# Optimization experiments

Hardware: AMD Instinct MI355X
Metric: run time of the kernel (lower is better)

## Reference

```python
import jax, jax.numpy as jnp
import numpy as np

N_USER = 200_000
N_ITEM = 100_000
E = 1_000_000
HID = 64
ED = 16      # edge_dim
DU = 128     # user feature dim
DI = 64      # item feature dim
NCONV = 4    # 2 layers x (fwd, rev)


def setup_inputs() -> dict:
    key = jax.random.key(0)
    ks = jax.random.split(key, 20)
    s = 0.1  # small init scale for numerical sanity
    return {
        'x_user': jax.random.normal(ks[0], (N_USER, DU), jnp.float32),
        'x_item': jax.random.normal(ks[1], (N_ITEM, DI), jnp.float32),
        'edge_attr': jax.random.normal(ks[2], (E, ED), jnp.float32),
        'src_idx': jax.random.randint(ks[3], (E,), 0, N_USER),
        'dst_idx': jax.random.randint(ks[4], (E,), 0, N_ITEM),
        # input projections
        'Wp_user': jax.random.normal(ks[5], (DU, HID), jnp.float32) * s,
        'bp_user': jnp.zeros((HID,), jnp.float32),
        'Wp_item': jax.random.normal(ks[6], (DI, HID), jnp.float32) * s,
        'bp_item': jnp.zeros((HID,), jnp.float32),
        # per-conv params, stacked over NCONV = [layer0 fwd, layer0 rev, layer1 fwd, layer1 rev]
        'eps': jnp.zeros((NCONV,), jnp.float32),  # train_eps=True, init 0
        'We': jax.random.normal(ks[7], (NCONV, ED, HID), jnp.float32) * s,
        'be': jnp.zeros((NCONV, HID), jnp.float32),
        'W1': jax.random.normal(ks[8], (NCONV, HID, HID), jnp.float32) * s,
        'b1': jnp.zeros((NCONV, HID), jnp.float32),
        'W2': jax.random.normal(ks[9], (NCONV, HID, HID), jnp.float32) * s,
        'b2': jnp.zeros((NCONV, HID), jnp.float32),
    }


def _gine(x_src, x_dst, e_src, e_dst, ea, eps, We, be, W1, b1, W2, b2):
    # GINEConv: out = MLP((1+eps)*x_dst + sum_j ReLU(x_src[j] + Lin(edge_attr_j)))
    msg = jax.nn.relu(x_src[e_src] + ea @ We + be)                 # [E, HID]
    agg = jax.ops.segment_sum(msg, e_dst, num_segments=x_dst.shape[0])
    h = (1.0 + eps) * x_dst + agg
    return jax.nn.relu(h @ W1 + b1) @ W2 + b2


def reference(x_user, x_item, edge_attr, src_idx, dst_idx,
              Wp_user, bp_user, Wp_item, bp_item,
              eps, We, be, W1, b1, W2, b2):
    h_u = jax.nn.relu(x_user @ Wp_user + bp_user)   # [N_USER, HID]
    h_i = jax.nn.relu(x_item @ Wp_item + bp_item)   # [N_ITEM, HID]
    for l in range(2):
        cf, cr = 2 * l, 2 * l + 1
        # fwd relation user->item (dst = item); rev = flipped edges, same edge_attr
        new_i = jax.nn.relu(_gine(h_u, h_i, src_idx, dst_idx, edge_attr,
                                  eps[cf], We[cf], be[cf], W1[cf], b1[cf], W2[cf], b2[cf]))
        new_u = jax.nn.relu(_gine(h_i, h_u, dst_idx, src_idx, edge_attr,
                                  eps[cr], We[cr], be[cr], W1[cr], b1[cr], W2[cr], b2[cr]))
        if l > 0:  # use_residual and not first layer
            h_u, h_i = h_u + new_u, h_i + new_i
        else:
            h_u, h_i = new_u, new_i
    return h_u, h_i
```

## Files before the change

kernel.cpp:

```cpp
#include <hip/hip_runtime.h>
#include <hip/hip_bf16.h>

typedef __hip_bfloat16 bf16;

#define N_USER 200000
#define N_ITEM 100000
#define NEDGE  1000000
#define HID    64

__device__ __forceinline__ float bf2f(unsigned int u) {
    unsigned int x = u << 16;
    float f; __builtin_memcpy(&f, &x, 4); return f;
}
__device__ __forceinline__ float ldf(const void* p, long i, int isf32) {
    if (isf32) return ((const float*)p)[i];
    return bf2f(((const unsigned short*)p)[i]);
}
__device__ __forceinline__ void stf(void* p, long i, int isf32, float v) {
    if (isf32) ((float*)p)[i] = v;
    else       ((bf16*)p)[i] = (bf16)v;
}
__device__ __forceinline__ void load_row16(const void* ea, long e, int isf32, float* v) {
    if (isf32) {
        const float4* p = (const float4*)((const float*)ea + e * 16);
        float4 a = p[0], b = p[1], c = p[2], d = p[3];
        v[0]=a.x; v[1]=a.y; v[2]=a.z; v[3]=a.w;
        v[4]=b.x; v[5]=b.y; v[6]=b.z; v[7]=b.w;
        v[8]=c.x; v[9]=c.y; v[10]=c.z; v[11]=c.w;
        v[12]=d.x; v[13]=d.y; v[14]=d.z; v[15]=d.w;
    } else {
        const int4* q = (const int4*)((const unsigned short*)ea + e * 16);
        int4 s0 = q[0], s1 = q[1];
        unsigned int w;
        w=(unsigned)s0.x; v[0]=bf2f(w & 0xffff); v[1]=bf2f(w >> 16);
        w=(unsigned)s0.y; v[2]=bf2f(w & 0xffff); v[3]=bf2f(w >> 16);
        w=(unsigned)s0.z; v[4]=bf2f(w & 0xffff); v[5]=bf2f(w >> 16);
        w=(unsigned)s0.w; v[6]=bf2f(w & 0xffff); v[7]=bf2f(w >> 16);
        w=(unsigned)s1.x; v[8]=bf2f(w & 0xffff); v[9]=bf2f(w >> 16);
        w=(unsigned)s1.y; v[10]=bf2f(w & 0xffff); v[11]=bf2f(w >> 16);
        w=(unsigned)s1.z; v[12]=bf2f(w & 0xffff); v[13]=bf2f(w >> 16);
        w=(unsigned)s1.w; v[14]=bf2f(w & 0xffff); v[15]=bf2f(w >> 16);
    }
}

__global__ void detect_kernel(const void* __restrict__ x, int* __restrict__ flag) {
    if (threadIdx.x == 0 && blockIdx.x == 0) {
        const unsigned short* p = (const unsigned short*)x;
        int f = 0;
        for (int i = 0; i < 512; i++) {
            int ex = (p[i] >> 7) & 0xFF;
            if (ex >= 137) f = 1;
        }
        *flag = f;
    }
}

__global__ __launch_bounds__(256) void hist_kernel(
    const int* __restrict__ key, int* __restrict__ cnt, int E)
{
    int e = blockIdx.x * 256 + threadIdx.x;
    if (e < E) atomicAdd(&cnt[key[e]], 1);
}

__global__ __launch_bounds__(1024) void scan_kernel(
    const int* __restrict__ deg, int* __restrict__ rowptr,
    int* __restrict__ cursor, int N)
{
    __shared__ int ssum[1024];
    __shared__ int s_carry;
    int tid = threadIdx.x;
    if (tid == 0) s_carry = 0;
    __syncthreads();
    for (int base = 0; base < N; base += 8192) {
        int i0 = base + tid * 8;
        int v[8]; int tot = 0;
#pragma unroll
        for (int k = 0; k < 8; k++) { int i = i0 + k; v[k] = (i < N) ? deg[i] : 0; tot += v[k]; }
        ssum[tid] = tot;
        __syncthreads();
        for (int off = 1; off < 1024; off <<= 1) {
            int t = (tid >= off) ? ssum[tid - off] : 0;
            __syncthreads();
            ssum[tid] += t;
            __syncthreads();
        }
        int exc = ssum[tid] - tot + s_carry;
#pragma unroll
        for (int k = 0; k < 8; k++) {
            int i = i0 + k;
            if (i < N) { rowptr[i] = exc; cursor[i] = exc; }
            exc += v[k];
        }
        __syncthreads();
        if (tid == 1023) s_carry += ssum[1023];
        __syncthreads();
    }
    if (tid == 0) rowptr[N] = s_carry;
}

__global__ __launch_bounds__(256) void scatter_kernel(
    const int* __restrict__ key, const int* __restrict__ other,
    int* __restrict__ cursor, int2* __restrict__ perm, int E)
{
    int e = blockIdx.x * 256 + threadIdx.x;
    if (e >= E) return;
    int p = atomicAdd(&cursor[key[e]], 1);
    perm[p] = make_int2(e, other[e]);
}

template<int K>
__global__ __launch_bounds__(256) void proj_kernel(
    const void* __restrict__ x, const void* __restrict__ W,
    const void* __restrict__ b, float* __restrict__ out, int N,
    const int* __restrict__ flagp)
{
    __shared__ float Ws[K * 64];
    __shared__ float xs[4][K];
    int isf32 = *flagp;
    int tid = threadIdx.x;
    for (int i = tid; i < K * 64; i += 256) Ws[i] = ldf(W, i, isf32);
    int r = tid >> 6, c = tid & 63;
    float bc = ldf(b, c, isf32);
    for (int row0 = blockIdx.x * 4; row0 < N; row0 += gridDim.x * 4) {
        __syncthreads();
        for (int i = tid; i < 4 * K; i += 256) {
            int rr = i / K, k = i - rr * K;
            int row = row0 + rr;
            xs[rr][k] = (row < N) ? ldf(x, (long)row * K + k, isf32) : 0.f;
        }
        __syncthreads();
        int row = row0 + r;
        float acc = bc;
#pragma unroll
        for (int k = 0; k < K; k++) acc = fmaf(xs[r][k], Ws[k * 64 + c], acc);
        if (row < N) out[(long)row * 64 + c] = fmaxf(acc, 0.f);
    }
}

template<int RESID>
__global__ __launch_bounds__(256, 4) void conv_kernel(
    const float* __restrict__ h_src, const float* __restrict__ h_dst,
    const int* __restrict__ rowptr, const int2* __restrict__ perm,
    const void* __restrict__ ea,
    const void* __restrict__ We, long weoff, const void* __restrict__ be, long beoff,
    const void* __restrict__ W1, const void* __restrict__ b1,
    const void* __restrict__ W2, const void* __restrict__ b2, long woff, long boff,
    const void* __restrict__ eps, int conv,
    float* __restrict__ outf, void* __restrict__ outv, long outoff,
    int N, const int* __restrict__ flagp)
{
    __shared__ float Wes[16 * 64];
    __shared__ float W1s[64 * 64];
    __shared__ float W2s[64 * 64];
    __shared__ float bes[64], b1s[64], b2s[64];
    __shared__ float vs[4][64], ts[4][64];
    int isf32 = *flagp;
    int tid = threadIdx.x;
    for (int i = tid; i < 4096; i += 256) {
        W1s[i] = ldf(W1, woff + i, isf32);
        W2s[i] = ldf(W2, woff + i, isf32);
    }
    for (int i = tid; i < 1024; i += 256) Wes[i] = ldf(We, weoff + i, isf32);
    if (tid < 64) {
        bes[tid] = ldf(be, beoff + tid, isf32);
        b1s[tid] = ldf(b1, boff + tid, isf32);
        b2s[tid] = ldf(b2, boff + tid, isf32);
    }
    __syncthreads();
    float eps1 = 1.f + ldf(eps, conv, isf32);
    int w = tid >> 6, c = tid & 63;

    for (int n0 = blockIdx.x * 4; n0 < N; n0 += gridDim.x * 4) {
        int n = n0 + w;
        float acc = 0.f, hv = 0.f;
        if (n < N) {
            hv = h_dst[(long)n * 64 + c];
            int jb = rowptr[n], je = rowptr[n + 1];
            int j = jb;
            for (; j + 4 <= je; j += 4) {
                int2 p0 = perm[j], p1 = perm[j+1], p2 = perm[j+2], p3 = perm[j+3];
                float a0[16], a1[16], a2[16], a3[16];
                load_row16(ea, p0.x, isf32, a0);
                load_row16(ea, p1.x, isf32, a1);
                load_row16(ea, p2.x, isf32, a2);
                load_row16(ea, p3.x, isf32, a3);
                float h0 = h_src[(long)p0.y * 64 + c];
                float h1 = h_src[(long)p1.y * 64 + c];
                float h2 = h_src[(long)p2.y * 64 + c];
                float h3 = h_src[(long)p3.y * 64 + c];
                float m0 = bes[c], m1 = m0, m2 = m0, m3 = m0;
#pragma unroll
                for (int k = 0; k < 16; k++) {
                    float wv = Wes[k * 64 + c];
                    m0 = fmaf(a0[k], wv, m0); m1 = fmaf(a1[k], wv, m1);
                    m2 = fmaf(a2[k], wv, m2); m3 = fmaf(a3[k], wv, m3);
                }
                acc += fmaxf(m0 + h0, 0.f); acc += fmaxf(m1 + h1, 0.f);
                acc += fmaxf(m2 + h2, 0.f); acc += fmaxf(m3 + h3, 0.f);
            }
            for (; j < je; j++) {
                int2 p0 = perm[j];
                float a0[16];
                load_row16(ea, p0.x, isf32, a0);
                float h0 = h_src[(long)p0.y * 64 + c];
                float m0 = bes[c];
#pragma unroll
                for (int k = 0; k < 16; k++) m0 = fmaf(a0[k], Wes[k * 64 + c], m0);
                acc += fmaxf(m0 + h0, 0.f);
            }
        }
        vs[w][c] = eps1 * hv + acc;
        __syncthreads();
        float t = b1s[c];
#pragma unroll
        for (int k = 0; k < 64; k++) t = fmaf(vs[w][k], W1s[k * 64 + c], t);
        t = fmaxf(t, 0.f);
        ts[w][c] = t;
        __syncthreads();
        float o = b2s[c];
#pragma unroll
        for (int k = 0; k < 64; k++) o = fmaf(ts[w][k], W2s[k * 64 + c], o);
        o = fmaxf(o, 0.f);
        if (n < N) {
            if (RESID) o += hv;
            long base = (long)n * 64;
            if (outv) stf(outv, outoff + base + c, isf32, o);
            else      outf[base + c] = o;
        }
    }
}

extern "C" void kernel_launch(void* const* d_in, const int* in_sizes, int n_in,
                              void* d_out, int out_size, void* d_ws, size_t ws_size,
                              hipStream_t stream)
{
    const void* x_user    = d_in[0];
    const void* x_item    = d_in[1];
    const void* edge_attr = d_in[2];
    const int*  src_idx   = (const int*)d_in[3];
    const int*  dst_idx   = (const int*)d_in[4];
    const void* Wp_user   = d_in[5];
    const void* bp_user   = d_in[6];
    const void* Wp_item   = d_in[7];
    const void* bp_item   = d_in[8];
    const void* eps       = d_in[9];
    const void* We        = d_in[10];
    const void* be        = d_in[11];
    const void* W1        = d_in[12];
    const void* b1        = d_in[13];
    const void* W2        = d_in[14];
    const void* b2        = d_in[15];

    float* ws   = (float*)d_ws;
    int*  flag  = (int*)d_ws;
    float* h_u  = ws + 256;
    float* h_i  = h_u + 12800000;
    float* h_u2 = h_i + 6400000;
    float* h_i2 = h_u2 + 12800000;
    int* rowptr_i = (int*)(h_i2 + 6400000);
    int* cursor_i = rowptr_i + 100096;
    int2* perm_i  = (int2*)(cursor_i + 100096);
    int* rowptr_u = (int*)(perm_i + 1000000);
    int* cursor_u = rowptr_u + 200192;
    int2* perm_u  = (int2*)(cursor_u + 200192);

    const int EG = (NEDGE + 255) / 256;

    detect_kernel<<<1, 64, 0, stream>>>(x_user, flag);

    hipMemsetAsync(cursor_i, 0, N_ITEM * sizeof(int), stream);
    hist_kernel<<<EG, 256, 0, stream>>>(dst_idx, cursor_i, NEDGE);
    scan_kernel<<<1, 1024, 0, stream>>>(cursor_i, rowptr_i, cursor_i, N_ITEM);
    scatter_kernel<<<EG, 256, 0, stream>>>(dst_idx, src_idx, cursor_i, perm_i, NEDGE);
    hipMemsetAsync(cursor_u, 0, N_USER * sizeof(int), stream);
    hist_kernel<<<EG, 256, 0, stream>>>(src_idx, cursor_u, NEDGE);
    scan_kernel<<<1, 1024, 0, stream>>>(cursor_u, rowptr_u, cursor_u, N_USER);
    scatter_kernel<<<EG, 256, 0, stream>>>(src_idx, dst_idx, cursor_u, perm_u, NEDGE);

    proj_kernel<128><<<1024, 256, 0, stream>>>(x_user, Wp_user, bp_user, h_u, N_USER, flag);
    proj_kernel<64><<<1024, 256, 0, stream>>>(x_item, Wp_item, bp_item, h_i, N_ITEM, flag);

    conv_kernel<0><<<1024, 256, 0, stream>>>(h_u, h_i, rowptr_i, perm_i, edge_attr,
        We, 0 * 1024, be, 0 * 64, W1, b1, W2, b2, 0 * 4096, 0 * 64,
        eps, 0, h_i2, nullptr, 0, N_ITEM, flag);
    conv_kernel<0><<<1024, 256, 0, stream>>>(h_i, h_u, rowptr_u, perm_u, edge_attr,
        We, 1 * 1024, be, 1 * 64, W1, b1, W2, b2, 1 * 4096, 1 * 64,
        eps, 1, h_u2, nullptr, 0, N_USER, flag);

    conv_kernel<1><<<1024, 256, 0, stream>>>(h_u2, h_i2, rowptr_i, perm_i, edge_attr,
        We, 2 * 1024, be, 2 * 64, W1, b1, W2, b2, 2 * 4096, 2 * 64,
        eps, 2, nullptr, d_out, (long)N_USER * HID, N_ITEM, flag);
    conv_kernel<1><<<1024, 256, 0, stream>>>(h_i2, h_u2, rowptr_u, perm_u, edge_attr,
        We, 3 * 1024, be, 3 * 64, W1, b1, W2, b2, 3 * 4096, 3 * 64,
        eps, 3, nullptr, d_out, 0, N_USER, flag);
}
```

Before: 2.393 ms.

## Store features bf16, pre-permute edge attrs, parallel scan, shuffle-based MLP

Intermediate node features are now stored in bf16 instead of fp32, which halves gather traffic. Edge attributes are converted to bf16 and written in CSR order during the scatter, so the conv kernel reads them contiguously instead of gathering by edge id. The single-block scans become a multi-block three-pass scan, the two histogram and scatter passes are merged into one, and the per-node MLP uses wave shuffles instead of shared memory and block barriers. The costs are extra precision loss in the stored activations and a larger workspace for the permuted edge attributes.

```diff
diff --git a/kernel.cpp b/kernel.cpp
--- a/kernel.cpp
+++ b/kernel.cpp
@@ -2,116 +2,143 @@
 #include <hip/hip_bf16.h>
 
 typedef __hip_bfloat16 bf16;
+typedef unsigned short ushort_t;
+typedef unsigned int uint_t;
 
 #define N_USER 200000
 #define N_ITEM 100000
 #define NEDGE  1000000
 #define HID    64
 
-__device__ __forceinline__ float bf2f(unsigned int u) {
-    unsigned int x = u << 16;
+__device__ __forceinline__ float bf2f(uint_t u) {
+    uint_t x = u << 16;
     float f; __builtin_memcpy(&f, &x, 4); return f;
+}
+__device__ __forceinline__ ushort_t f2bf(float f) {
+    bf16 h = (bf16)f;
+    ushort_t u; __builtin_memcpy(&u, &h, 2); return u;
 }
 __device__ __forceinline__ float ldf(const void* p, long i, int isf32) {
     if (isf32) return ((const float*)p)[i];
-    return bf2f(((const unsigned short*)p)[i]);
+    return bf2f(((const ushort_t*)p)[i]);
 }
 __device__ __forceinline__ void stf(void* p, long i, int isf32, float v) {
     if (isf32) ((float*)p)[i] = v;
-    else       ((bf16*)p)[i] = (bf16)v;
-}
-__device__ __forceinline__ void load_row16(const void* ea, long e, int isf32, float* v) {
-    if (isf32) {
-        const float4* p = (const float4*)((const float*)ea + e * 16);
-        float4 a = p[0], b = p[1], c = p[2], d = p[3];
-        v[0]=a.x; v[1]=a.y; v[2]=a.z; v[3]=a.w;
-        v[4]=b.x; v[5]=b.y; v[6]=b.z; v[7]=b.w;
-        v[8]=c.x; v[9]=c.y; v[10]=c.z; v[11]=c.w;
-        v[12]=d.x; v[13]=d.y; v[14]=d.z; v[15]=d.w;
-    } else {
-        const int4* q = (const int4*)((const unsigned short*)ea + e * 16);
-        int4 s0 = q[0], s1 = q[1];
-        unsigned int w;
-        w=(unsigned)s0.x; v[0]=bf2f(w & 0xffff); v[1]=bf2f(w >> 16);
-        w=(unsigned)s0.y; v[2]=bf2f(w & 0xffff); v[3]=bf2f(w >> 16);
-        w=(unsigned)s0.z; v[4]=bf2f(w & 0xffff); v[5]=bf2f(w >> 16);
-        w=(unsigned)s0.w; v[6]=bf2f(w & 0xffff); v[7]=bf2f(w >> 16);
-        w=(unsigned)s1.x; v[8]=bf2f(w & 0xffff); v[9]=bf2f(w >> 16);
-        w=(unsigned)s1.y; v[10]=bf2f(w & 0xffff); v[11]=bf2f(w >> 16);
-        w=(unsigned)s1.z; v[12]=bf2f(w & 0xffff); v[13]=bf2f(w >> 16);
-        w=(unsigned)s1.w; v[14]=bf2f(w & 0xffff); v[15]=bf2f(w >> 16);
-    }
-}
-
-__global__ void detect_kernel(const void* __restrict__ x, int* __restrict__ flag) {
+    else       ((ushort_t*)p)[i] = f2bf(v);
+}
+
+__global__ void detect_kernel(const ushort_t* __restrict__ x, int* __restrict__ flag) {
+    int t = threadIdx.x;
+    int f = 0;
+#pragma unroll
+    for (int k = 0; k < 4; k++) {
+        int ex = (x[t * 4 + k] >> 7) & 0xFF;
+        f |= (ex >= 137);
+    }
+    unsigned long long b = __ballot(f);
+    if (t == 0) *flag = (b != 0ULL) ? 1 : 0;
+}
+
+__global__ __launch_bounds__(256) void hist_kernel(
+    const int* __restrict__ src, const int* __restrict__ dst,
+    int* __restrict__ cnt_i, int* __restrict__ cnt_u, int E)
+{
+    int e = blockIdx.x * 256 + threadIdx.x;
+    if (e < E) {
+        atomicAdd(&cnt_i[dst[e]], 1);
+        atomicAdd(&cnt_u[src[e]], 1);
+    }
+}
+
+__global__ __launch_bounds__(1024) void scan_block_kernel(
+    const int* __restrict__ deg, int* __restrict__ local,
+    int* __restrict__ partials, int N)
+{
+    __shared__ int ssum[1024];
+    int b = blockIdx.x, tid = threadIdx.x;
+    int i0 = b * 8192 + tid * 8;
+    int v[8]; int tot = 0;
+#pragma unroll
+    for (int k = 0; k < 8; k++) { int i = i0 + k; v[k] = (i < N) ? deg[i] : 0; tot += v[k]; }
+    ssum[tid] = tot;
+    __syncthreads();
+    for (int off = 1; off < 1024; off <<= 1) {
+        int t = (tid >= off) ? ssum[tid - off] : 0;
+        __syncthreads();
+        ssum[tid] += t;
+        __syncthreads();
+    }
+    int exc = ssum[tid] - tot;
+#pragma unroll
+    for (int k = 0; k < 8; k++) { int i = i0 + k; if (i < N) local[i] = exc; exc += v[k]; }
+    if (tid == 1023) partials[b] = ssum[1023];
+}
+
+__global__ void scan_partials_kernel(int* __restrict__ partials,
+                                     int* __restrict__ rowptrN, int nb)
+{
     if (threadIdx.x == 0 && blockIdx.x == 0) {
-        const unsigned short* p = (const unsigned short*)x;
-        int f = 0;
-        for (int i = 0; i < 512; i++) {
-            int ex = (p[i] >> 7) & 0xFF;
-            if (ex >= 137) f = 1;
-        }
-        *flag = f;
-    }
-}
-
-__global__ __launch_bounds__(256) void hist_kernel(
-    const int* __restrict__ key, int* __restrict__ cnt, int E)
-{
-    int e = blockIdx.x * 256 + threadIdx.x;
-    if (e < E) atomicAdd(&cnt[key[e]], 1);
-}
-
-__global__ __launch_bounds__(1024) void scan_kernel(
-    const int* __restrict__ deg, int* __restrict__ rowptr,
+        int a = 0;
+        for (int i = 0; i < nb; i++) { int t = partials[i]; partials[i] = a; a += t; }
+        *rowptrN = a;
+    }
+}
+
+__global__ __launch_bounds__(1024) void scan_add_kernel(
+    const int* __restrict__ partials, int* __restrict__ rowptr,
     int* __restrict__ cursor, int N)
 {
-    __shared__ int ssum[1024];
-    __shared__ int s_carry;
-    int tid = threadIdx.x;
-    if (tid == 0) s_carry = 0;
-    __syncthreads();
-    for (int base = 0; base < N; base += 8192) {
-        int i0 = base + tid * 8;
-        int v[8]; int tot = 0;
-#pragma unroll
-        for (int k = 0; k < 8; k++) { int i = i0 + k; v[k] = (i < N) ? deg[i] : 0; tot += v[k]; }
-        ssum[tid] = tot;
-        __syncthreads();
-        for (int off = 1; off < 1024; off <<= 1) {
-            int t = (tid >= off) ? ssum[tid - off] : 0;
-            __syncthreads();
-            ssum[tid] += t;
-            __syncthreads();
-        }
-        int exc = ssum[tid] - tot + s_carry;
-#pragma unroll
-        for (int k = 0; k < 8; k++) {
-            int i = i0 + k;
-            if (i < N) { rowptr[i] = exc; cursor[i] = exc; }
-            exc += v[k];
-        }
-        __syncthreads();
-        if (tid == 1023) s_carry += ssum[1023];
-        __syncthreads();
-    }
-    if (tid == 0) rowptr[N] = s_carry;
+    int b = blockIdx.x, tid = threadIdx.x;
+    int i0 = b * 8192 + tid * 8;
+    int p = partials[b];
+#pragma unroll
+    for (int k = 0; k < 8; k++) {
+        int i = i0 + k;
+        if (i < N) { int v = rowptr[i] + p; rowptr[i] = v; cursor[i] = v; }
+    }
 }
 
 __global__ __launch_bounds__(256) void scatter_kernel(
-    const int* __restrict__ key, const int* __restrict__ other,
-    int* __restrict__ cursor, int2* __restrict__ perm, int E)
+    const int* __restrict__ src, const int* __restrict__ dst,
+    const void* __restrict__ ea,
+    int* __restrict__ cur_i, int* __restrict__ cur_u,
+    int* __restrict__ perm_i, int* __restrict__ perm_u,
+    ushort_t* __restrict__ eap_i, ushort_t* __restrict__ eap_u,
+    int E, const int* __restrict__ flagp)
 {
     int e = blockIdx.x * 256 + threadIdx.x;
     if (e >= E) return;
-    int p = atomicAdd(&cursor[key[e]], 1);
-    perm[p] = make_int2(e, other[e]);
+    int isf32 = *flagp;
+    uint4 r0, r1;
+    if (isf32) {
+        const float4* p = (const float4*)((const float*)ea + (long)e * 16);
+        float4 f0 = p[0], f1 = p[1], f2 = p[2], f3 = p[3];
+        ushort_t h[16];
+        h[0]=f2bf(f0.x); h[1]=f2bf(f0.y); h[2]=f2bf(f0.z); h[3]=f2bf(f0.w);
+        h[4]=f2bf(f1.x); h[5]=f2bf(f1.y); h[6]=f2bf(f1.z); h[7]=f2bf(f1.w);
+        h[8]=f2bf(f2.x); h[9]=f2bf(f2.y); h[10]=f2bf(f2.z); h[11]=f2bf(f2.w);
+        h[12]=f2bf(f3.x); h[13]=f2bf(f3.y); h[14]=f2bf(f3.z); h[15]=f2bf(f3.w);
+        __builtin_memcpy(&r0, h, 16);
+        __builtin_memcpy(&r1, h + 8, 16);
+    } else {
+        const uint4* p = (const uint4*)((const ushort_t*)ea + (long)e * 16);
+        r0 = p[0]; r1 = p[1];
+    }
+    int s = src[e], d = dst[e];
+    int pi = atomicAdd(&cur_i[d], 1);
+    perm_i[pi] = s;
+    uint4* qi = (uint4*)(eap_i + (long)pi * 16);
+    qi[0] = r0; qi[1] = r1;
+    int pu = atomicAdd(&cur_u[s], 1);
+    perm_u[pu] = d;
+    uint4* qu = (uint4*)(eap_u + (long)pu * 16);
+    qu[0] = r0; qu[1] = r1;
 }
 
 template<int K>
 __global__ __launch_bounds__(256) void proj_kernel(
     const void* __restrict__ x, const void* __restrict__ W,
-    const void* __restrict__ b, float* __restrict__ out, int N,
+    const void* __restrict__ b, ushort_t* __restrict__ out, int N,
     const int* __restrict__ flagp)
 {
     __shared__ float Ws[K * 64];
@@ -133,100 +160,104 @@
         float acc = bc;
 #pragma unroll
         for (int k = 0; k < K; k++) acc = fmaf(xs[r][k], Ws[k * 64 + c], acc);
-        if (row < N) out[(long)row * 64 + c] = fmaxf(acc, 0.f);
-    }
+        if (row < N) out[(long)row * 64 + c] = f2bf(fmaxf(acc, 0.f));
+    }
+}
+
+__device__ __forceinline__ float row_fma(uint4 A, uint4 B,
+                                         const float* __restrict__ Wes,
+                                         int c, float m)
+{
+    uint_t u;
+    u = A.x; m = fmaf(bf2f(u & 0xffff), Wes[0*64+c], m);  m = fmaf(bf2f(u >> 16), Wes[1*64+c], m);
+    u = A.y; m = fmaf(bf2f(u & 0xffff), Wes[2*64+c], m);  m = fmaf(bf2f(u >> 16), Wes[3*64+c], m);
+    u = A.z; m = fmaf(bf2f(u & 0xffff), Wes[4*64+c], m);  m = fmaf(bf2f(u >> 16), Wes[5*64+c], m);
+    u = A.w; m = fmaf(bf2f(u & 0xffff), Wes[6*64+c], m);  m = fmaf(bf2f(u >> 16), Wes[7*64+c], m);
+    u = B.x; m = fmaf(bf2f(u & 0xffff), Wes[8*64+c], m);  m = fmaf(bf2f(u >> 16), Wes[9*64+c], m);
+    u = B.y; m = fmaf(bf2f(u & 0xffff), Wes[10*64+c], m); m = fmaf(bf2f(u >> 16), Wes[11*64+c], m);
+    u = B.z; m = fmaf(bf2f(u & 0xffff), Wes[12*64+c], m); m = fmaf(bf2f(u >> 16), Wes[13*64+c], m);
+    u = B.w; m = fmaf(bf2f(u & 0xffff), Wes[14*64+c], m); m = fmaf(bf2f(u >> 16), Wes[15*64+c], m);
+    return m;
 }
 
 template<int RESID>
-__global__ __launch_bounds__(256, 4) void conv_kernel(
-    const float* __restrict__ h_src, const float* __restrict__ h_dst,
-    const int* __restrict__ rowptr, const int2* __restrict__ perm,
-    const void* __restrict__ ea,
-    const void* __restrict__ We, long weoff, const void* __restrict__ be, long beoff,
+__global__ __launch_bounds__(512, 8) void conv_kernel(
+    const ushort_t* __restrict__ h_src, const ushort_t* __restrict__ h_dst,
+    const int* __restrict__ rowptr, const int* __restrict__ perm,
+    const ushort_t* __restrict__ eap,
+    const void* __restrict__ We, const void* __restrict__ be,
     const void* __restrict__ W1, const void* __restrict__ b1,
-    const void* __restrict__ W2, const void* __restrict__ b2, long woff, long boff,
+    const void* __restrict__ W2, const void* __restrict__ b2,
     const void* __restrict__ eps, int conv,
-    float* __restrict__ outf, void* __restrict__ outv, long outoff,
+    ushort_t* __restrict__ outh, void* __restrict__ outv, long outoff,
     int N, const int* __restrict__ flagp)
 {
     __shared__ float Wes[16 * 64];
     __shared__ float W1s[64 * 64];
     __shared__ float W2s[64 * 64];
     __shared__ float bes[64], b1s[64], b2s[64];
-    __shared__ float vs[4][64], ts[4][64];
     int isf32 = *flagp;
     int tid = threadIdx.x;
-    for (int i = tid; i < 4096; i += 256) {
+    long woff = (long)conv * 4096, weoff = (long)conv * 1024, boff = (long)conv * 64;
+    for (int i = tid; i < 4096; i += 512) {
         W1s[i] = ldf(W1, woff + i, isf32);
         W2s[i] = ldf(W2, woff + i, isf32);
     }
-    for (int i = tid; i < 1024; i += 256) Wes[i] = ldf(We, weoff + i, isf32);
+    for (int i = tid; i < 1024; i += 512) Wes[i] = ldf(We, weoff + i, isf32);
     if (tid < 64) {
-        bes[tid] = ldf(be, beoff + tid, isf32);
+        bes[tid] = ldf(be, boff + tid, isf32);
         b1s[tid] = ldf(b1, boff + tid, isf32);
         b2s[tid] = ldf(b2, boff + tid, isf32);
     }
     __syncthreads();
     float eps1 = 1.f + ldf(eps, conv, isf32);
-    int w = tid >> 6, c = tid & 63;
-
-    for (int n0 = blockIdx.x * 4; n0 < N; n0 += gridDim.x * 4) {
-        int n = n0 + w;
-        float acc = 0.f, hv = 0.f;
-        if (n < N) {
-            hv = h_dst[(long)n * 64 + c];
-            int jb = rowptr[n], je = rowptr[n + 1];
-            int j = jb;
-            for (; j + 4 <= je; j += 4) {
-                int2 p0 = perm[j], p1 = perm[j+1], p2 = perm[j+2], p3 = perm[j+3];
-                float a0[16], a1[16], a2[16], a3[16];
-                load_row16(ea, p0.x, isf32, a0);
-                load_row16(ea, p1.x, isf32, a1);
-                load_row16(ea, p2.x, isf32, a2);
-                load_row16(ea, p3.x, isf32, a3);
-                float h0 = h_src[(long)p0.y * 64 + c];
-                float h1 = h_src[(long)p1.y * 64 + c];
-                float h2 = h_src[(long)p2.y * 64 + c];
-                float h3 = h_src[(long)p3.y * 64 + c];
-                float m0 = bes[c], m1 = m0, m2 = m0, m3 = m0;
-#pragma unroll
-                for (int k = 0; k < 16; k++) {
-                    float wv = Wes[k * 64 + c];
-                    m0 = fmaf(a0[k], wv, m0); m1 = fmaf(a1[k], wv, m1);
-                    m2 = fmaf(a2[k], wv, m2); m3 = fmaf(a3[k], wv, m3);
-                }
-                acc += fmaxf(m0 + h0, 0.f); acc += fmaxf(m1 + h1, 0.f);
-                acc += fmaxf(m2 + h2, 0.f); acc += fmaxf(m3 + h3, 0.f);
-            }
-            for (; j < je; j++) {
-                int2 p0 = perm[j];
-                float a0[16];
-                load_row16(ea, p0.x, isf32, a0);
-                float h0 = h_src[(long)p0.y * 64 + c];
-                float m0 = bes[c];
-#pragma unroll
-                for (int k = 0; k < 16; k++) m0 = fmaf(a0[k], Wes[k * 64 + c], m0);
-                acc += fmaxf(m0 + h0, 0.f);
-            }
+    int c = tid & 63;
+    int wave = blockIdx.x * 8 + (tid >> 6);
+    int nwaves = gridDim.x * 8;
+
+    for (int n = wave; n < N; n += nwaves) {
+        float hv = bf2f(h_dst[(long)n * 64 + c]);
+        int jb = rowptr[n], je = rowptr[n + 1];
+        float acc = 0.f;
+        float bec = bes[c];
+        int j = jb;
+        for (; j + 4 <= je; j += 4) {
+            int s0 = perm[j], s1 = perm[j + 1], s2 = perm[j + 2], s3 = perm[j + 3];
+            float h0 = bf2f(h_src[(long)s0 * 64 + c]);
+            float h1 = bf2f(h_src[(long)s1 * 64 + c]);
+            float h2 = bf2f(h_src[(long)s2 * 64 + c]);
+            float h3 = bf2f(h_src[(long)s3 * 64 + c]);
+            const uint4* q = (const uint4*)(eap + (long)j * 16);
+            uint4 A, B;
+            float m0 = bec, m1 = bec, m2 = bec, m3 = bec;
+            A = q[0]; B = q[1]; m0 = row_fma(A, B, Wes, c, m0);
+            A = q[2]; B = q[3]; m1 = row_fma(A, B, Wes, c, m1);
+            A = q[4]; B = q[5]; m2 = row_fma(A, B, Wes, c, m2);
+            A = q[6]; B = q[7]; m3 = row_fma(A, B, Wes, c, m3);
+            acc += fmaxf(m0 + h0, 0.f) + fmaxf(m1 + h1, 0.f)
+                 + fmaxf(m2 + h2, 0.f) + fmaxf(m3 + h3, 0.f);
         }
-        vs[w][c] = eps1 * hv + acc;
-        __syncthreads();
+        for (; j < je; j++) {
+            int s0 = perm[j];
+            float h0 = bf2f(h_src[(long)s0 * 64 + c]);
+            const uint4* q = (const uint4*)(eap + (long)j * 16);
+            uint4 A = q[0], B = q[1];
+            float m0 = row_fma(A, B, Wes, c, bec);
+            acc += fmaxf(m0 + h0, 0.f);
+        }
+        float v = eps1 * hv + acc;
         float t = b1s[c];
 #pragma unroll
-        for (int k = 0; k < 64; k++) t = fmaf(vs[w][k], W1s[k * 64 + c], t);
+        for (int k = 0; k < 64; k++) t = fmaf(__shfl(v, k, 64), W1s[k * 64 + c], t);
         t = fmaxf(t, 0.f);
-        ts[w][c] = t;
-        __syncthreads();
         float o = b2s[c];
 #pragma unroll
-        for (int k = 0; k < 64; k++) o = fmaf(ts[w][k], W2s[k * 64 + c], o);
+        for (int k = 0; k < 64; k++) o = fmaf(__shfl(t, k, 64), W2s[k * 64 + c], o);
         o = fmaxf(o, 0.f);
-        if (n < N) {
-            if (RESID) o += hv;
-            long base = (long)n * 64;
-            if (outv) stf(outv, outoff + base + c, isf32, o);
-            else      outf[base + c] = o;
-        }
+        if (RESID) o += hv;
+        long base = (long)n * 64 + c;
+        if (outh) outh[base] = f2bf(o);
+        else      stf(outv, outoff + base, isf32, o);
     }
 }
 
@@ -251,46 +282,51 @@
     const void* W2        = d_in[14];
     const void* b2        = d_in[15];
 
-    float* ws   = (float*)d_ws;
-    int*  flag  = (int*)d_ws;
-    float* h_u  = ws + 256;
-    float* h_i  = h_u + 12800000;
-    float* h_u2 = h_i + 6400000;
-    float* h_i2 = h_u2 + 12800000;
-    int* rowptr_i = (int*)(h_i2 + 6400000);
-    int* cursor_i = rowptr_i + 100096;
-    int2* perm_i  = (int2*)(cursor_i + 100096);
-    int* rowptr_u = (int*)(perm_i + 1000000);
-    int* cursor_u = rowptr_u + 200192;
-    int2* perm_u  = (int2*)(cursor_u + 200192);
-
-    const int EG = (NEDGE + 255) / 256;
-
-    detect_kernel<<<1, 64, 0, stream>>>(x_user, flag);
-
-    hipMemsetAsync(cursor_i, 0, N_ITEM * sizeof(int), stream);
-    hist_kernel<<<EG, 256, 0, stream>>>(dst_idx, cursor_i, NEDGE);
-    scan_kernel<<<1, 1024, 0, stream>>>(cursor_i, rowptr_i, cursor_i, N_ITEM);
-    scatter_kernel<<<EG, 256, 0, stream>>>(dst_idx, src_idx, cursor_i, perm_i, NEDGE);
-    hipMemsetAsync(cursor_u, 0, N_USER * sizeof(int), stream);
-    hist_kernel<<<EG, 256, 0, stream>>>(src_idx, cursor_u, NEDGE);
-    scan_kernel<<<1, 1024, 0, stream>>>(cursor_u, rowptr_u, cursor_u, N_USER);
-    scatter_kernel<<<EG, 256, 0, stream>>>(src_idx, dst_idx, cursor_u, perm_u, NEDGE);
+    char* W = (char*)d_ws;
+    int*      flag     = (int*)W;
+    ushort_t* h_u      = (ushort_t*)(W + 1024);
+    ushort_t* h_i      = (ushort_t*)(W + 25601024);
+    ushort_t* h_u2     = (ushort_t*)(W + 38401024);
+    ushort_t* h_i2     = (ushort_t*)(W + 64001024);
+    int*      rowptr_i = (int*)(W + 76801024);
+    int*      rowptr_u = (int*)(W + 77201408);
+    int*      cursor_i = (int*)(W + 78001664);
+    int*      cursor_u = (int*)(W + 78401664);
+    int*      perm_i   = (int*)(W + 79201664);
+    int*      perm_u   = (int*)(W + 83201664);
+    ushort_t* eap_i    = (ushort_t*)(W + 87201664);
+    ushort_t* eap_u    = (ushort_t*)(W + 119201664);
+    int*      part_i   = (int*)(W + 151201664);
+    int*      part_u   = (int*)(W + 151201920);
+
+    const int EG   = (NEDGE + 255) / 256;
+    const int NB_I = (N_ITEM + 8191) / 8192;
+    const int NB_U = (N_USER + 8191) / 8192;
+
+    detect_kernel<<<1, 64, 0, stream>>>((const ushort_t*)x_user, flag);
+
+    hipMemsetAsync(cursor_i, 0, (size_t)(N_ITEM + N_USER) * sizeof(int), stream);
+    hist_kernel<<<EG, 256, 0, stream>>>(src_idx, dst_idx, cursor_i, cursor_u, NEDGE);
+    scan_block_kernel<<<NB_I, 1024, 0, stream>>>(cursor_i, rowptr_i, part_i, N_ITEM);
+    scan_partials_kernel<<<1, 64, 0, stream>>>(part_i, rowptr_i + N_ITEM, NB_I);
+    scan_add_kernel<<<NB_I, 1024, 0, stream>>>(part_i, rowptr_i, cursor_i, N_ITEM);
+    scan_block_kernel<<<NB_U, 1024, 0, stream>>>(cursor_u, rowptr_u, part_u, N_USER);
+    scan_partials_kernel<<<1, 64, 0, stream>>>(part_u, rowptr_u + N_USER, NB_U);
+    scan_add_kernel<<<NB_U, 1024, 0, stream>>>(part_u, rowptr_u, cursor_u, N_USER);
+    scatter_kernel<<<EG, 256, 0, stream>>>(src_idx, dst_idx, edge_attr,
+                                           cursor_i, cursor_u, perm_i, perm_u,
+                                           eap_i, eap_u, NEDGE, flag);
 
     proj_kernel<128><<<1024, 256, 0, stream>>>(x_user, Wp_user, bp_user, h_u, N_USER, flag);
     proj_kernel<64><<<1024, 256, 0, stream>>>(x_item, Wp_item, bp_item, h_i, N_ITEM, flag);
 
-    conv_kernel<0><<<1024, 256, 0, stream>>>(h_u, h_i, rowptr_i, perm_i, edge_attr,
-        We, 0 * 1024, be, 0 * 64, W1, b1, W2, b2, 0 * 4096, 0 * 64,
-        eps, 0, h_i2, nullptr, 0, N_ITEM, flag);
-    conv_kernel<0><<<1024, 256, 0, stream>>>(h_i, h_u, rowptr_u, perm_u, edge_attr,
-        We, 1 * 1024, be, 1 * 64, W1, b1, W2, b2, 1 * 4096, 1 * 64,
-        eps, 1, h_u2, nullptr, 0, N_USER, flag);
-
-    conv_kernel<1><<<1024, 256, 0, stream>>>(h_u2, h_i2, rowptr_i, perm_i, edge_attr,
-        We, 2 * 1024, be, 2 * 64, W1, b1, W2, b2, 2 * 4096, 2 * 64,
-        eps, 2, nullptr, d_out, (long)N_USER * HID, N_ITEM, flag);
-    conv_kernel<1><<<1024, 256, 0, stream>>>(h_i2, h_u2, rowptr_u, perm_u, edge_attr,
-        We, 3 * 1024, be, 3 * 64, W1, b1, W2, b2, 3 * 4096, 3 * 64,
-        eps, 3, nullptr, d_out, 0, N_USER, flag);
-}
+    conv_kernel<0><<<1024, 512, 0, stream>>>(h_u, h_i, rowptr_i, perm_i, eap_i,
+        We, be, W1, b1, W2, b2, eps, 0, h_i2, nullptr, 0, N_ITEM, flag);
+    conv_kernel<0><<<1024, 512, 0, stream>>>(h_i, h_u, rowptr_u, perm_u, eap_u,
+        We, be, W1, b1, W2, b2, eps, 1, h_u2, nullptr, 0, N_USER, flag);
+
+    conv_kernel<1><<<1024, 512, 0, stream>>>(h_u2, h_i2, rowptr_i, perm_i, eap_i,
+        We, be, W1, b1, W2, b2, eps, 2, nullptr, d_out, (long)N_USER * HID, N_ITEM, flag);
+    conv_kernel<1><<<1024, 512, 0, stream>>>(h_i2, h_u2, rowptr_u, perm_u, eap_u,
+        We, be, W1, b1, W2, b2, eps, 3, nullptr, d_out, 0, N_USER, flag);
+}
```

After: 6.645 ms. +177.7%, slower.
